# Optimization experiments

Measured on AMD Instinct MI355X. Metric: run time of the kernel, lower is better.

The kernel has to match this reference:

```python
import jax, jax.numpy as jnp
import numpy as np

N, D, K, G = 262144, 256, 1024, 4
C = D // G
BETA = 0.5


def setup_inputs() -> dict:
    key = jax.random.key(0)
    k1, k2 = jax.random.split(key)
    z = jax.random.normal(k1, (N, D), dtype=jnp.float32)
    # original init: uniform(-1/K, 1/K)
    codebooks = jax.random.uniform(k2, (G, K, C), dtype=jnp.float32,
                                   minval=-1.0 / K, maxval=1.0 / K)
    return {"z": z, "codebooks": codebooks}


def reference(z, codebooks):
    # z: [N, D] -> [N, G, C]; codebooks: [G, K, C]
    zg = z.reshape(-1, G, C)
    # squared distances: ||z||^2 + ||e||^2 - 2 z.e  -> [N, G, K]
    z_sq = jnp.sum(zg ** 2, axis=-1, keepdims=True)            # [N, G, 1]
    e_sq = jnp.sum(codebooks ** 2, axis=-1)                    # [G, K]
    dots = jnp.einsum('ngc,gkc->ngk', zg, codebooks)           # [N, G, K]
    d = z_sq + e_sq[None, :, :] - 2.0 * dots
    idx = jnp.argmin(d, axis=-1)                               # [N, G]
    # gather codes: [N, G, C]
    zq = codebooks[jnp.arange(G)[None, :], idx]
    # per-group VQ loss, averaged over groups (means over N and C per group)
    sg = jax.lax.stop_gradient
    commit = jnp.mean((sg(zq) - zg) ** 2, axis=(0, 2))         # [G]
    embed = jnp.mean((zq - sg(zg)) ** 2, axis=(0, 2))          # [G]
    loss = jnp.mean(BETA * commit + embed)
    # straight-through estimator
    zq_st = zg + sg(zq - zg)
    return zq_st.reshape(-1, D), loss
```

## Files before the change

### kernel.cpp

```cpp
#include <hip/hip_runtime.h>
#include <hip/hip_fp16.h>
#include <stdint.h>

typedef _Float16 f16;
typedef f16   f16x8 __attribute__((ext_vector_type(8)));
typedef float f32x4 __attribute__((ext_vector_type(4)));

#define NTOK 262144
#define DDIM 256
#define KCB  1024
#define GG   4
#define CC   64
#define FR   4
#define ROWS_PER_BLK (FR * 16 * 4)
#define NBLKX (NTOK / ROWS_PER_BLK)
#define NPART (NBLKX * GG)
#define TILE_K 64
#define NTILE  (KCB / TILE_K)
#define TILE_B (TILE_K * CC * 2)

static __device__ __forceinline__ uint32_t umin32(uint32_t a, uint32_t b) { return a < b ? a : b; }

typedef __attribute__((address_space(1))) const void gv_t;
typedef __attribute__((address_space(3))) void lv_t;
static __device__ __forceinline__ void gl_lds16(const void* g, void* l) {
    __builtin_amdgcn_global_load_lds((gv_t*)g, (lv_t*)l, 16, 0, 0);
}
static __device__ __forceinline__ void gl_lds4(const void* g, void* l) {
    __builtin_amdgcn_global_load_lds((gv_t*)g, (lv_t*)l, 4, 0, 0);
}

__global__ __launch_bounds__(64) void vq_prep(const float* __restrict__ cb,
                                              f16* __restrict__ cb16,
                                              float* __restrict__ esq05) {
    int gk = blockIdx.x;
    int c  = threadIdx.x;
    float v = cb[(size_t)gk * CC + c];
    cb16[(size_t)gk * CC + c] = (f16)v;
    float s = v * v;
    #pragma unroll
    for (int off = 32; off; off >>= 1) s += __shfl_down(s, off, 64);
    if (c == 0) esq05[gk] = 0.5f + s;
}

__global__ __launch_bounds__(256, 4) void vq_argmin(const float* __restrict__ z,
                                                    const f16* __restrict__ cb16,
                                                    const float* __restrict__ esq05,
                                                    unsigned short* __restrict__ idx,
                                                    float* __restrict__ part) {
    const int lane = threadIdx.x & 63;
    const int w    = threadIdx.x >> 6;
    const int g    = blockIdx.y;
    const int r0   = blockIdx.x * ROWS_PER_BLK + w * (FR * 16);
    const int q    = lane >> 4;
    const int t    = lane & 15;

    __shared__ __align__(16) char sb[2][TILE_B + 256];
    __shared__ float ls[4];

    const f16*   cbg = cb16  + (size_t)g * KCB * CC;
    const float* eg  = esq05 + (size_t)g * KCB;

    #define STAGE(tile, bufsel)                                                      \
        do {                                                                         \
            const char* gtile = (const char*)cbg + (size_t)(tile) * TILE_B;          \
            _Pragma("unroll")                                                        \
            for (int c2 = 0; c2 < 2; ++c2) {                                         \
                uint32_t x  = (uint32_t)(w * 2048 + c2 * 1024 + lane * 16);          \
                uint32_t gx = x ^ (((x >> 7) & 7u) << 4);                            \
                gl_lds16(gtile + gx, &sb[bufsel][w * 2048 + c2 * 1024]);             \
            }                                                                        \
            if (w == 0) gl_lds4(eg + (tile) * TILE_K + lane, &sb[bufsel][TILE_B]);   \
        } while (0)

    STAGE(0, 0);

    f16x8 a[FR][2];
    float zsq[FR];
    #pragma unroll
    for (int f = 0; f < FR; ++f) {
        int row = r0 + f * 16 + t;
        const float* zp = z + (size_t)row * DDIM + g * CC + q * 8;
        float4 v0 = *(const float4*)(zp);
        float4 v1 = *(const float4*)(zp + 4);
        float4 v2 = *(const float4*)(zp + 32);
        float4 v3 = *(const float4*)(zp + 36);
        f16x8 a0 = { (f16)(-2.f*v0.x),(f16)(-2.f*v0.y),(f16)(-2.f*v0.z),(f16)(-2.f*v0.w),
                     (f16)(-2.f*v1.x),(f16)(-2.f*v1.y),(f16)(-2.f*v1.z),(f16)(-2.f*v1.w) };
        f16x8 a1 = { (f16)(-2.f*v2.x),(f16)(-2.f*v2.y),(f16)(-2.f*v2.z),(f16)(-2.f*v2.w),
                     (f16)(-2.f*v3.x),(f16)(-2.f*v3.y),(f16)(-2.f*v3.z),(f16)(-2.f*v3.w) };
        a[f][0] = a0; a[f][1] = a1;
        float s = v0.x*v0.x + v0.y*v0.y + v0.z*v0.z + v0.w*v0.w
                + v1.x*v1.x + v1.y*v1.y + v1.z*v1.z + v1.w*v1.w
                + v2.x*v2.x + v2.y*v2.y + v2.z*v2.z + v2.w*v2.w
                + v3.x*v3.x + v3.y*v3.y + v3.z*v3.z + v3.w*v3.w;
        s += __shfl_xor(s, 16, 64);
        s += __shfl_xor(s, 32, 64);
        zsq[f] = s;
    }

    uint32_t run[FR][4];
    #pragma unroll
    for (int f = 0; f < FR; ++f)
        #pragma unroll
        for (int i = 0; i < 4; ++i) run[f][i] = 0xFFFFFFFFu;

    const uint32_t binner = (uint32_t)t * 128 + (((uint32_t)(q * 16)) ^ (((uint32_t)(t & 7)) << 4));

    for (int tt = 0; tt < NTILE; ++tt) {
        __syncthreads();
        if (tt + 1 < NTILE) STAGE(tt + 1, (tt + 1) & 1);
        const char*  bb = sb[tt & 1];
        const float* eb = (const float*)(sb[tt & 1] + TILE_B);
        #pragma unroll
        for (int sub = 0; sub < 4; ++sub) {
            f16x8 b0 = *(const f16x8*)(bb + sub * 2048 + binner);
            f16x8 b1 = *(const f16x8*)(bb + sub * 2048 + (binner ^ 64));
            float e  = eb[sub * 16 + t];
            f32x4 ce = { e, e, e, e };
            uint32_t code = (uint32_t)(tt * TILE_K + sub * 16 + t);
            f32x4 acc[FR];
            __builtin_amdgcn_s_setprio(1);
            #pragma unroll
            for (int f = 0; f < FR; ++f)
                acc[f] = __builtin_amdgcn_mfma_f32_16x16x32_f16(a[f][0], b0, ce, 0, 0, 0);
            #pragma unroll
            for (int f = 0; f < FR; ++f)
                acc[f] = __builtin_amdgcn_mfma_f32_16x16x32_f16(a[f][1], b1, acc[f], 0, 0, 0);
            __builtin_amdgcn_s_setprio(0);
            #pragma unroll
            for (int f = 0; f < FR; ++f) {
                #pragma unroll
                for (int i = 0; i < 4; ++i) {
                    uint32_t k = (__float_as_uint(acc[f][i]) & 0xFFFFFC00u) | code;
                    run[f][i] = umin32(run[f][i], k);
                }
            }
        }
    }

    float lsum = 0.0f;
    #pragma unroll
    for (int f = 0; f < FR; ++f) {
        #pragma unroll
        for (int i = 0; i < 4; ++i) {
            uint32_t k = run[f][i];
            k = umin32(k, __shfl_xor(k, 1, 64));
            k = umin32(k, __shfl_xor(k, 2, 64));
            k = umin32(k, __shfl_xor(k, 4, 64));
            k = umin32(k, __shfl_xor(k, 8, 64));
            int   kw     = (int)(k & 1023u);
            float minval = __uint_as_float(k & 0xFFFFFC00u) - 0.5f;
            int rloc = q * 4 + i;
            int grow = r0 + f * 16 + rloc;
            float zs = __shfl(zsq[f], rloc, 64);
            if (t == 0) {
                idx[(grow << 2) | g] = (unsigned short)kw;
                lsum += zs + minval;
            }
        }
    }
    #pragma unroll
    for (int off = 32; off; off >>= 1) lsum += __shfl_down(lsum, off, 64);

    if (lane == 0) ls[w] = lsum;
    __syncthreads();
    if (threadIdx.x == 0) {
        part[blockIdx.y * NBLKX + blockIdx.x] = ls[0] + ls[1] + ls[2] + ls[3];
    }
}

__global__ __launch_bounds__(256) void vq_gather(const unsigned short* __restrict__ idx,
                                                 const float* __restrict__ cb32,
                                                 float* __restrict__ out) {
    const int stride = gridDim.x * 256;
    const int total  = NTOK * (DDIM / 4);
    for (int i = blockIdx.x * 256 + threadIdx.x; i < total; i += stride) {
        int row = i >> 6;
        int d4  = i & 63;
        int g   = d4 >> 4;
        int c4  = d4 & 15;
        int k   = idx[(row << 2) | g];
        float4 v = *(const float4*)(cb32 + (size_t)(((g << 10) + k) << 6) + (c4 << 2));
        *(float4*)(out + ((size_t)row << 8) + (d4 << 2)) = v;
    }
}

__global__ __launch_bounds__(256) void vq_final(const float* __restrict__ part,
                                                float* __restrict__ out_loss) {
    __shared__ float ls[4];
    float s = 0.0f;
    for (int i = threadIdx.x; i < NPART; i += 256) s += part[i];
    #pragma unroll
    for (int off = 32; off; off >>= 1) s += __shfl_down(s, off, 64);
    int lane = threadIdx.x & 63, w = threadIdx.x >> 6;
    if (lane == 0) ls[w] = s;
    __syncthreads();
    if (threadIdx.x == 0) {
        *out_loss = 1.5f * (ls[0] + ls[1] + ls[2] + ls[3]) * (1.0f / ((float)NTOK * (float)DDIM));
    }
}

extern "C" void kernel_launch(void* const* d_in, const int* in_sizes, int n_in,
                              void* d_out, int out_size, void* d_ws, size_t ws_size,
                              hipStream_t stream) {
    const float* z  = (const float*)d_in[0];
    const float* cb = (const float*)d_in[1];
    float* out = (float*)d_out;

    char* ws = (char*)d_ws;
    f16*   cb16  = (f16*)ws;
    float* esq05 = (float*)(ws + (size_t)GG * KCB * CC * sizeof(f16));
    float* part  = (float*)(ws + 512*1024 + 16*1024);
    unsigned short* idx = (unsigned short*)(ws + 512*1024 + 32*1024);

    vq_prep<<<GG * KCB, 64, 0, stream>>>(cb, cb16, esq05);

    dim3 grid(NBLKX, GG);
    vq_argmin<<<grid, 256, 0, stream>>>(z, cb16, esq05, idx, part);

    vq_gather<<<4096, 256, 0, stream>>>(idx, cb, out);

    vq_final<<<1, 256, 0, stream>>>(part, out + (size_t)NTOK * DDIM);
}
```

Measured before the change: 233.2 us.

## Load whole group codebook into LDS once per 1024-thread block, drop per-tile syncs

```diff
diff --git a/kernel.cpp b/kernel.cpp
--- a/kernel.cpp
+++ b/kernel.cpp
@@ -12,12 +12,11 @@
 #define GG   4
 #define CC   64
 #define FR   4
-#define ROWS_PER_BLK (FR * 16 * 4)
+#define WAVES 16
+#define ROWS_PER_BLK (FR * 16 * WAVES)
 #define NBLKX (NTOK / ROWS_PER_BLK)
 #define NPART (NBLKX * GG)
-#define TILE_K 64
-#define NTILE  (KCB / TILE_K)
-#define TILE_B (TILE_K * CC * 2)
+#define CBB   (KCB * CC * 2)
 
 static __device__ __forceinline__ uint32_t umin32(uint32_t a, uint32_t b) { return a < b ? a : b; }
 
@@ -43,37 +42,32 @@
     if (c == 0) esq05[gk] = 0.5f + s;
 }
 
-__global__ __launch_bounds__(256, 4) void vq_argmin(const float* __restrict__ z,
-                                                    const f16* __restrict__ cb16,
-                                                    const float* __restrict__ esq05,
-                                                    unsigned short* __restrict__ idx,
-                                                    float* __restrict__ part) {
-    const int lane = threadIdx.x & 63;
-    const int w    = threadIdx.x >> 6;
+__global__ __launch_bounds__(1024, 4) void vq_argmin(const float* __restrict__ z,
+                                                     const f16* __restrict__ cb16,
+                                                     const float* __restrict__ esq05,
+                                                     unsigned short* __restrict__ idx,
+                                                     float* __restrict__ part) {
+    const int tid  = threadIdx.x;
+    const int lane = tid & 63;
+    const int w    = tid >> 6;
     const int g    = blockIdx.y;
     const int r0   = blockIdx.x * ROWS_PER_BLK + w * (FR * 16);
     const int q    = lane >> 4;
     const int t    = lane & 15;
 
-    __shared__ __align__(16) char sb[2][TILE_B + 256];
-    __shared__ float ls[4];
+    __shared__ __align__(16) char sb[CBB + KCB * 4];
+    __shared__ float ls[WAVES];
 
     const f16*   cbg = cb16  + (size_t)g * KCB * CC;
     const float* eg  = esq05 + (size_t)g * KCB;
 
-    #define STAGE(tile, bufsel)                                                      \
-        do {                                                                         \
-            const char* gtile = (const char*)cbg + (size_t)(tile) * TILE_B;          \
-            _Pragma("unroll")                                                        \
-            for (int c2 = 0; c2 < 2; ++c2) {                                         \
-                uint32_t x  = (uint32_t)(w * 2048 + c2 * 1024 + lane * 16);          \
-                uint32_t gx = x ^ (((x >> 7) & 7u) << 4);                            \
-                gl_lds16(gtile + gx, &sb[bufsel][w * 2048 + c2 * 1024]);             \
-            }                                                                        \
-            if (w == 0) gl_lds4(eg + (tile) * TILE_K + lane, &sb[bufsel][TILE_B]);   \
-        } while (0)
-
-    STAGE(0, 0);
+    #pragma unroll
+    for (int c = 0; c < 8; ++c) {
+        uint32_t x  = (uint32_t)(c * 16384 + w * 1024 + lane * 16);
+        uint32_t gx = x ^ (((x >> 7) & 7u) << 4);
+        gl_lds16((const char*)cbg + gx, &sb[c * 16384 + w * 1024]);
+    }
+    gl_lds4(eg + tid, &sb[CBB + w * 256]);
 
     f16x8 a[FR][2];
     float zsq[FR];
@@ -107,36 +101,37 @@
 
     const uint32_t binner = (uint32_t)t * 128 + (((uint32_t)(q * 16)) ^ (((uint32_t)(t & 7)) << 4));
 
-    for (int tt = 0; tt < NTILE; ++tt) {
-        __syncthreads();
-        if (tt + 1 < NTILE) STAGE(tt + 1, (tt + 1) & 1);
-        const char*  bb = sb[tt & 1];
-        const float* eb = (const float*)(sb[tt & 1] + TILE_B);
-        #pragma unroll
-        for (int sub = 0; sub < 4; ++sub) {
-            f16x8 b0 = *(const f16x8*)(bb + sub * 2048 + binner);
-            f16x8 b1 = *(const f16x8*)(bb + sub * 2048 + (binner ^ 64));
-            float e  = eb[sub * 16 + t];
-            f32x4 ce = { e, e, e, e };
-            uint32_t code = (uint32_t)(tt * TILE_K + sub * 16 + t);
-            f32x4 acc[FR];
-            __builtin_amdgcn_s_setprio(1);
+    __syncthreads();
+
+    const float* eb = (const float*)(sb + CBB);
+
+    #pragma unroll 2
+    for (int s = 0; s < 64; s += 2) {
+        const char* pA = sb + (size_t)s * 2048;
+        f16x8 b0A = *(const f16x8*)(pA + binner);
+        f16x8 b1A = *(const f16x8*)(pA + (binner ^ 64));
+        f16x8 b0B = *(const f16x8*)(pA + 2048 + binner);
+        f16x8 b1B = *(const f16x8*)(pA + 2048 + (binner ^ 64));
+        float eA = eb[s * 16 + t];
+        float eB = eb[s * 16 + 16 + t];
+        f32x4 ceA = { eA, eA, eA, eA };
+        f32x4 ceB = { eB, eB, eB, eB };
+        uint32_t codeA = (uint32_t)(s * 16 + t);
+        __builtin_amdgcn_s_setprio(1);
+        #pragma unroll
+        for (int f = 0; f < FR; ++f) {
+            f32x4 accA = __builtin_amdgcn_mfma_f32_16x16x32_f16(a[f][0], b0A, ceA, 0, 0, 0);
+            accA = __builtin_amdgcn_mfma_f32_16x16x32_f16(a[f][1], b1A, accA, 0, 0, 0);
+            f32x4 accB = __builtin_amdgcn_mfma_f32_16x16x32_f16(a[f][0], b0B, ceB, 0, 0, 0);
+            accB = __builtin_amdgcn_mfma_f32_16x16x32_f16(a[f][1], b1B, accB, 0, 0, 0);
             #pragma unroll
-            for (int f = 0; f < FR; ++f)
-                acc[f] = __builtin_amdgcn_mfma_f32_16x16x32_f16(a[f][0], b0, ce, 0, 0, 0);
-            #pragma unroll
-            for (int f = 0; f < FR; ++f)
-                acc[f] = __builtin_amdgcn_mfma_f32_16x16x32_f16(a[f][1], b1, acc[f], 0, 0, 0);
-            __builtin_amdgcn_s_setprio(0);
-            #pragma unroll
-            for (int f = 0; f < FR; ++f) {
-                #pragma unroll
-                for (int i = 0; i < 4; ++i) {
-                    uint32_t k = (__float_as_uint(acc[f][i]) & 0xFFFFFC00u) | code;
-                    run[f][i] = umin32(run[f][i], k);
-                }
+            for (int i = 0; i < 4; ++i) {
+                uint32_t kA = (__float_as_uint(accA[i]) & 0xFFFFFC00u) | codeA;
+                uint32_t kB = (__float_as_uint(accB[i]) & 0xFFFFFC00u) | (codeA + 16);
+                run[f][i] = umin32(run[f][i], umin32(kA, kB));
             }
         }
+        __builtin_amdgcn_s_setprio(0);
     }
 
     float lsum = 0.0f;
@@ -165,8 +160,11 @@
 
     if (lane == 0) ls[w] = lsum;
     __syncthreads();
-    if (threadIdx.x == 0) {
-        part[blockIdx.y * NBLKX + blockIdx.x] = ls[0] + ls[1] + ls[2] + ls[3];
+    if (tid == 0) {
+        float s = 0.0f;
+        #pragma unroll
+        for (int i = 0; i < WAVES; ++i) s += ls[i];
+        part[blockIdx.y * NBLKX + blockIdx.x] = s;
     }
 }
 
@@ -217,7 +215,7 @@
     vq_prep<<<GG * KCB, 64, 0, stream>>>(cb, cb16, esq05);
 
     dim3 grid(NBLKX, GG);
-    vq_argmin<<<grid, 256, 0, stream>>>(z, cb16, esq05, idx, part);
+    vq_argmin<<<grid, 1024, 0, stream>>>(z, cb16, esq05, idx, part);
 
     vq_gather<<<4096, 256, 0, stream>>>(idx, cb, out);
 
```

Measured after the change: 272.8 us. 1.17x slower.
